# Performance work log

Measured on AMD Instinct MI355X. Metric: run time of the kernel, lower is better.

The kernel has to match this reference:

```python
import jax, jax.numpy as jnp
from jax import lax
import numpy as np

NF = 64      # feature channels
G = 8        # mask groups
NBR = 3      # top-k neighbors
PATCH = 7    # correlation patch size (patches[0])
CORK = 3     # correlation / unfold kernel size
PAD_COR = 1  # (CORK-1)//2
PAD_S = 4    # PAD_COR + (PATCH-1)//2
ADD = 6      # 2*PAD_S - CORK + 1
B, H, W = 4, 96, 96


def leaky(x):
    return jnp.where(x >= 0, x, 0.1 * x)


def _conv(x, w, b, pad):
    y = lax.conv_general_dilated(x, w, (1, 1), [(pad[0], pad[0]), (pad[1], pad[1])],
                                 dimension_numbers=('NCHW', 'OIHW', 'NCHW'))
    return y + b[None, :, None, None]


def _normalize(x, eps=1e-12):
    n = jnp.sqrt(jnp.sum(x * x, axis=1, keepdims=True))
    return x / jnp.maximum(n, eps)


def _correlation(f1, f2):
    # spatial-correlation-sampler: kernel=3, patch=7, stride=1, pad=1, dilations=1
    # out[b, ph*7+pw, i, j] = sum_{c,u,v} f1p[b,c,i+u,j+v] * f2p[b,c,i+u+ph-3, j+v+pw-3]
    # (unnormalized; only topk indices are consumed downstream, so any positive
    #  constant scale is irrelevant)
    Bx, C, Hx, Wx = f1.shape
    f1p = jnp.pad(f1, ((0, 0), (0, 0), (PAD_COR, PAD_COR), (PAD_COR, PAD_COR)))
    f2p = jnp.pad(f2, ((0, 0), (0, 0), (PAD_S, PAD_S), (PAD_S, PAD_S)))
    outs = []
    for ph in range(PATCH):
        for pw in range(PATCH):
            s = jnp.sum(f1p * f2p[:, :, ph:ph + Hx + 2, pw:pw + Wx + 2], axis=1)  # [B,H+2,W+2]
            o = sum(s[:, u:u + Hx, v:v + Wx] for u in range(CORK) for v in range(CORK))
            outs.append(o)
    return jnp.stack(outs, axis=1)  # [B, 49, H, W]


def setup_inputs() -> dict:
    key = jax.random.key(0)
    ks = jax.random.split(key, 16)

    def wt(k, shape):
        fan_in = shape[1] * shape[2] * shape[3]
        return jax.random.normal(k, shape, jnp.float32) * (1.0 / np.sqrt(fan_in))

    return {
        'ref_fea_l': jax.random.normal(ks[0], (B, NF, H, W), jnp.float32),
        'w1': wt(ks[1], (NF, NF * 2, 3, 3)), 'b1': jnp.zeros((NF,), jnp.float32),
        'w2': wt(ks[2], (NF, NF, 3, 3)),     'b2': jnp.zeros((NF,), jnp.float32),
        'w3': wt(ks[3], (NF, NF, 7, 1)),     'b3': jnp.zeros((NF,), jnp.float32),
        'w4': wt(ks[4], (NF, NF, 1, 7)),     'b4': jnp.zeros((NF,), jnp.float32),
        'wm': wt(ks[5], (G * CORK ** 2, NF, 3, 3)), 'bm': jnp.zeros((G * CORK ** 2,), jnp.float32),
        'wnn': wt(ks[6], (NF, NF * NBR, 3, 3)), 'bnn': jnp.zeros((NF,), jnp.float32),
        'wf': wt(ks[7], (NF, NF * 2, 3, 3)),    'bf': jnp.zeros((NF,), jnp.float32),
    }


def reference(ref_fea_l, w1, b1, w2, b2, w3, b3, w4, b4, wm, bm, wnn, bnn, wf, bf):
    Bx, C, Hx, Wx = ref_fea_l.shape
    nbr_fea = ref_fea_l  # aliased in the original forward

    # mask branch
    x = jnp.concatenate([nbr_fea, ref_fea_l], axis=1)
    x = leaky(_conv(x, w1, b1, (1, 1)))
    x = leaky(_conv(x, w2, b2, (1, 1)))
    x = leaky(_conv(x, w3, b3, (3, 0)))
    x = leaky(_conv(x, w4, b4, (0, 3)))
    mask = _conv(x, wm, bm, (1, 1)).reshape(Bx, G, 1, CORK ** 2, Hx, Wx)

    # correlation + topk neighbor displacements
    nref = _normalize(ref_fea_l)
    corr = _correlation(nref, nref)                     # [B,49,H,W]
    _, idx = lax.top_k(corr.transpose(0, 2, 3, 1), NBR)  # [B,H,W,NBR]

    # flat indices into the (H+6)x(W+6) unfold grid
    ph = idx // PATCH
    pw = idx % PATCH
    yy = jnp.arange(Hx)[:, None, None]
    xx = jnp.arange(Wx)[None, :, None]
    flat = ((ph + yy) * (Wx + ADD) + (pw + xx)).reshape(Bx, Hx * Wx * NBR)

    # unfold (im2col) of nbr features with pad 4, then gather chosen 3x3 patches
    nbr_pad = jnp.pad(nbr_fea, ((0, 0), (0, 0), (PAD_S, PAD_S), (PAD_S, PAD_S)))
    patches = lax.conv_general_dilated_patches(nbr_pad, (CORK, CORK), (1, 1), 'VALID',
                                               dimension_numbers=('NCHW', 'OIHW', 'NCHW'))
    pl = patches.reshape(Bx, C * CORK ** 2, -1).transpose(0, 2, 1)  # [B, (H+6)(W+6), C*9]
    gath = jnp.take_along_axis(pl, flat[:, :, None], axis=1)        # [B, HW*NBR, C*9]
    gath = gath.reshape(Bx * Hx * Wx, NBR * C, CORK, CORK)

    # conv over gathered patches then modulated mask-weighted reduce
    g = leaky(_conv(gath, wnn, bnn, (1, 1)))                         # [BHW, C, 3, 3]
    g = g.reshape(Bx, Hx, Wx, C, CORK ** 2).transpose(0, 3, 4, 1, 2)
    g = g.reshape(Bx, G, C // G, CORK ** 2, Hx, Wx)
    agg = leaky(jnp.sum(g * mask, axis=3).reshape(Bx, C, Hx, Wx))

    out = leaky(_conv(jnp.concatenate([ref_fea_l, agg], axis=1), wf, bf, (1, 1)))
    return out
```

## Files before the change

### kernel.cpp

```cpp
#include <hip/hip_runtime.h>
#include <hip/hip_bf16.h>

constexpr int BATCH = 4;
constexpr int H = 96, W = 96, HW = H * W;
constexpr int NBR = 3;

using bf16x8 = __attribute__((ext_vector_type(8))) short;
using f32x4 = __attribute__((ext_vector_type(4))) float;

static __device__ __forceinline__ float leakyf(float x) {
    return x >= 0.f ? x : 0.1f * x;
}

static __device__ __forceinline__ short f2bf(float x) {
    __hip_bfloat16 h = __float2bfloat16(x);
    return *reinterpret_cast<short*>(&h);
}

static __device__ __forceinline__ float bf2f(short s) {
    __hip_bfloat16 h = *reinterpret_cast<__hip_bfloat16*>(&s);
    return __bfloat162float(h);
}

__global__ __launch_bounds__(256) void k_pre(const float* __restrict__ ref,
                                             short* __restrict__ reft,
                                             float* __restrict__ nrn) {
    int p = blockIdx.x * 256 + threadIdx.x;
    if (p >= BATCH * HW) return;
    int b = p / HW, ij = p % HW;
    const float* src = ref + b * 64 * HW + ij;
    float v[64];
    float ss = 0.f;
#pragma unroll
    for (int c = 0; c < 64; ++c) {
        v[c] = src[c * HW];
        ss += v[c] * v[c];
    }
    float inv = 1.f / fmaxf(sqrtf(ss), 1e-12f);
    short* rd = reft + (size_t)p * 64;
#pragma unroll
    for (int cc = 0; cc < 8; ++cc) {
        bf16x8 o;
#pragma unroll
        for (int j = 0; j < 8; ++j) o[j] = f2bf(v[cc * 8 + j]);
        *(bf16x8*)(rd + cc * 8) = o;
    }
    float* nd = nrn + b * 64 * HW + ij;
#pragma unroll
    for (int c = 0; c < 64; ++c) nd[c * HW] = v[c] * inv;
}

__global__ void k_prep(const float* __restrict__ src, short* __restrict__ dst,
                       int OC, int ICt, int ICsrc, int KH, int KW, int NT,
                       int fold, int total) {
    int i = blockIdx.x * 256 + threadIdx.x;
    if (i >= total) return;
    int e = i & 7, l = (i >> 3) & 63;
    int rest = i >> 9;
    int nt = rest % NT;
    rest /= NT;
    int ICK = ICt >> 5;
    int kk = rest % ICK;
    int tap = rest / ICK;
    int ic = kk * 32 + (l >> 4) * 8 + e;
    int oc = nt * 16 + (l & 15);
    int u = tap / KW, v = tap % KW;
    float val = 0.f;
    if (oc < OC) {
        val = src[((oc * ICsrc + ic) * KH + u) * KW + v];
        if (fold) val += src[((oc * ICsrc + 64 + ic) * KH + u) * KW + v];
    }
    dst[i] = f2bf(val);
}

template <int KH, int KW, int IC, int OC, int OMODE, bool BLDS, int NSPL>
__global__ __launch_bounds__(512) void k_cmfma(
    const short* __restrict__ inA, const short* __restrict__ inB,
    const short* __restrict__ Bp, const float* __restrict__ bias,
    void* __restrict__ outp) {
    constexpr int TI = 8, TJ = 32;
    constexpr int PH = (KH - 1) / 2, PW = (KW - 1) / 2;
    constexpr int LR = TI + KH - 1, LC = TJ + KW - 1;
    constexpr int ICB = IC * 2;
    constexpr int LS = (ICB == 128) ? 7 : 8;
    constexpr int ICK = IC / 32;
    constexpr int NTF = (OC + 15) / 16;
    constexpr int NTb = NTF / NSPL;
    constexpr int TAPS = KH * KW;
    constexpr int NOCT = ICB / 16;
    __shared__ char Xs[LR * LC * ICB];
    __shared__ short Bs[BLDS ? TAPS * ICK * NTb * 512 : 8];
    const int tj0 = blockIdx.x * TJ, ti0 = blockIdx.y * TI;
    const int b = blockIdx.z / NSPL;
    const int nt0 = (blockIdx.z % NSPL) * NTb;
    const int tid = threadIdx.x;
    if (BLDS) {
        for (int u2 = tid; u2 < TAPS * ICK * NTb * 64; u2 += 512) {
            int l2 = u2 & 63;
            int rest = u2 >> 6;
            int nt = rest % NTb;
            int qk = rest / NTb;
            ((bf16x8*)Bs)[u2] = ((const bf16x8*)Bp)[(qk * NTF + nt0 + nt) * 64 + l2];
        }
    }
    for (int u2 = tid; u2 < LR * LC * NOCT; u2 += 512) {
        int oct = u2 % NOCT;
        int hp = u2 / NOCT;
        int hr = hp / LC, hc = hp % LC;
        int gi = ti0 + hr - PH, gj = tj0 + hc - PW;
        bf16x8 v = {};
        if (gi >= 0 && gi < H && gj >= 0 && gj < W) {
            const short* s = (oct < 8) ? inA : inB;
            v = *(const bf16x8*)(s + (size_t)(b * HW + gi * W + gj) * 64 +
                                 (oct & 7) * 8);
        }
        int byte = hp * ICB + oct * 16;
        byte ^= ((byte >> LS) & 7) << 4;
        *(bf16x8*)(Xs + byte) = v;
    }
    __syncthreads();
    const int wave = tid >> 6, l = tid & 63;
    const int r = l & 15, q = l >> 4;
    const int mt0 = wave * 2;
    int p0 = mt0 * 16 + r, p1 = p0 + 16;
    int li0 = p0 >> 5, lj0 = p0 & 31, li1 = p1 >> 5, lj1 = p1 & 31;
    f32x4 acc[2][NTb] = {};
#pragma unroll
    for (int t = 0; t < TAPS; ++t) {
        const int u = t / KW, v = t % KW;
        int hp0 = (li0 + u) * LC + (lj0 + v);
        int hp1 = (li1 + u) * LC + (lj1 + v);
#pragma unroll
        for (int kk = 0; kk < ICK; ++kk) {
            int ab0 = hp0 * ICB + kk * 64 + q * 16;
            ab0 ^= ((ab0 >> LS) & 7) << 4;
            int ab1 = hp1 * ICB + kk * 64 + q * 16;
            ab1 ^= ((ab1 >> LS) & 7) << 4;
            bf16x8 a0 = *(const bf16x8*)(Xs + ab0);
            bf16x8 a1 = *(const bf16x8*)(Xs + ab1);
            const short* bbase =
                BLDS ? (const short*)Bs + (t * ICK + kk) * NTb * 512 + l * 8
                     : Bp + ((t * ICK + kk) * NTF + nt0) * 512 + l * 8;
#pragma unroll
            for (int nt = 0; nt < NTb; ++nt) {
                bf16x8 bv = *(const bf16x8*)(bbase + nt * 512);
                acc[0][nt] =
                    __builtin_amdgcn_mfma_f32_16x16x32_bf16(a0, bv, acc[0][nt], 0, 0, 0);
                acc[1][nt] =
                    __builtin_amdgcn_mfma_f32_16x16x32_bf16(a1, bv, acc[1][nt], 0, 0, 0);
            }
        }
    }
    const int col = l & 15;
#pragma unroll
    for (int mt = 0; mt < 2; ++mt)
#pragma unroll
        for (int nt = 0; nt < NTb; ++nt) {
            int oc = (nt0 + nt) * 16 + col;
            float bs = (oc < OC) ? bias[oc] : 0.f;
#pragma unroll
            for (int j = 0; j < 4; ++j) {
                int p = (mt0 + mt) * 16 + q * 4 + j;
                int gi = ti0 + (p >> 5), gj = tj0 + (p & 31);
                float val = acc[mt][nt][j] + bs;
                if (OMODE == 0) {
                    val = leakyf(val);
                    *((short*)outp + (size_t)(b * HW + gi * W + gj) * 64 + oc) =
                        f2bf(val);
                } else if (OMODE == 1) {
                    if (oc < 72)
                        *((short*)outp + (size_t)(b * HW + gi * W + gj) * 72 + oc) =
                            f2bf(val);
                } else {
                    val = leakyf(val);
                    *((float*)outp + (size_t)(b * 64 + oc) * HW + gi * W + gj) = val;
                }
            }
        }
}

__global__ void k_corr_sym(const float* __restrict__ nr, float* __restrict__ S) {
    int idx = blockIdx.x * 256 + threadIdx.x;
    if (idx >= BATCH * 25 * 98 * 98) return;
    int x = idx % 98;
    int y = (idx / 98) % 98;
    int d = (idx / (98 * 98)) % 25;
    int b = idx / (98 * 98 * 25);
    int dy = d / 7, dx = d % 7;
    int f1i = y - 1, f1j = x - 1;
    int f2i = y + dy - 4, f2j = x + dx - 4;
    float r = 0.f;
    if (f1i >= 0 && f1i < H && f1j >= 0 && f1j < W && f2i >= 0 && f2i < H &&
        f2j >= 0 && f2j < W) {
        const float* p1 = nr + b * 64 * HW + f1i * W + f1j;
        const float* p2 = nr + b * 64 * HW + f2i * W + f2j;
#pragma unroll 16
        for (int c = 0; c < 64; ++c) r = fmaf(p1[c * HW], p2[c * HW], r);
    }
    S[((size_t)(b * 49 + d)) * (98 * 98) + y * 98 + x] = r;
    if (d < 24) {
        int y2 = y + dy - 3, x2 = x + dx - 3;
        if (y2 >= 0 && y2 < 98 && x2 >= 0 && x2 < 98)
            S[((size_t)(b * 49 + 48 - d)) * (98 * 98) + y2 * 98 + x2] = r;
    }
}

__global__ void k_topk(const float* __restrict__ S, int* __restrict__ idx3) {
    int p = blockIdx.x * 256 + threadIdx.x;
    if (p >= BATCH * HW) return;
    int b = p / HW, i = (p % HW) / W, j = p % W;
    float v0 = -1e30f, v1 = -1e30f, v2 = -1e30f;
    int d0 = 0, d1 = 0, d2 = 0;
    for (int d = 0; d < 49; ++d) {
        const float* s = S + ((b * 49 + d) * 98 + i) * 98 + j;
        float v = 0.f;
#pragma unroll
        for (int u = 0; u < 3; ++u)
#pragma unroll
            for (int vv = 0; vv < 3; ++vv) v += s[u * 98 + vv];
        if (v > v0) {
            v2 = v1; d2 = d1; v1 = v0; d1 = d0; v0 = v; d0 = d;
        } else if (v > v1) {
            v2 = v1; d2 = d1; v1 = v; d1 = d;
        } else if (v > v2) {
            v2 = v; d2 = d;
        }
    }
    idx3[p * 3 + 0] = d0;
    idx3[p * 3 + 1] = d1;
    idx3[p * 3 + 2] = d2;
}

__global__ void k_bswz2(const float* __restrict__ wnn, short* __restrict__ B2) {
    int i = blockIdx.x * 256 + threadIdx.x;
    if (i >= 4 * 3 * 2 * 9 * 512) return;
    int e = i & 7, l = (i >> 3) & 63;
    int t = (i >> 9) % 9;
    int h2 = (i / (512 * 9)) % 2;
    int n = (i / (512 * 9 * 2)) % 3;
    int nt = i / (512 * 9 * 2 * 3);
    int oc = nt * 16 + (l & 15);
    int c = h2 * 32 + (l >> 4) * 8 + e;
    int u = t / 3, v = t % 3;
    B2[i] = f2bf(wnn[((oc * 192 + n * 64 + c) * 3 + u) * 3 + v]);
}

__global__ __launch_bounds__(512, 4) void k_agg_mfma(
    const short* __restrict__ refT, const int* __restrict__ idx3,
    const short* __restrict__ B2, const float* __restrict__ bnn,
    const short* __restrict__ maskT, short* __restrict__ agg) {
    constexpr int PX = 32;
    constexpr int BUFB = 2 * 18 * 64 * 8 * 2;
    __shared__ short A_lds[2 * 2 * 18 * 64 * 8];
    __shared__ int sd[PX][NBR];
    const int p0 = blockIdx.x * PX;
    const int b = p0 / HW;
    const int i0 = (p0 % HW) / W;
    const int j0 = p0 % W;
    const int tid = threadIdx.x;
    if (tid < PX * NBR)
        sd[tid / NBR][tid % NBR] = idx3[(p0 + tid / NBR) * NBR + tid % NBR];
    __syncthreads();

    bf16x8 greg[5];
    int gbyte[5];

    auto LD = [&](int n, int buf) {
#pragma unroll
        for (int i = 0; i < 5; ++i) {
            int u = tid + i * 512;
            if (u < PX * 9 * 8) {
                int oct = u & 7;
                int q = u >> 3;
                int rs = q % 9;
                int px = q / 9;
                int d = sd[px][n];
                int gi = i0 + d / 7 + rs / 3 - 4;
                int gj = j0 + px + d % 7 + rs % 3 - 4;
                bf16x8 val = {};
                if (gi >= 0 && gi < H && gj >= 0 && gj < W)
                    val = *(const bf16x8*)(refT +
                                           (size_t)(b * HW + gi * W + gj) * 64 +
                                           oct * 8);
                int kkl = rs * 2 + (oct >> 2);
                int chunk = ((px >> 4) * 18 + kkl) * 64 + (oct & 3) * 16 + (px & 15);
                int byte = buf * BUFB + (chunk << 4);
                byte ^= ((byte >> 8) & 7) << 4;
                greg[i] = val;
                gbyte[i] = byte;
            } else {
                gbyte[i] = -1;
            }
        }
    };
    auto WR = [&]() {
#pragma unroll
        for (int i = 0; i < 5; ++i)
            if (gbyte[i] >= 0) *(bf16x8*)((char*)A_lds + gbyte[i]) = greg[i];
    };

    const int wave = tid >> 6;
    const int lane = tid & 63;
    const int w = wave & 3;
    const int half = wave >> 2;
    f32x4 acc[9] = {};
    const short* Bw = B2 + (size_t)w * (3 * 2 * 9 * 512) + lane * 8;

    auto COMPUTE = [&](int n, int buf) {
#pragma unroll
        for (int h2 = 0; h2 < 2; ++h2) {
            const short* bb = Bw + (n * 2 + h2) * 9 * 512;
            bf16x8 bv[9];
#pragma unroll
            for (int t = 0; t < 9; ++t) bv[t] = *(const bf16x8*)(bb + t * 512);
#pragma unroll
            for (int rs = 0; rs < 9; ++rs) {
                int kkl = rs * 2 + h2;
                int ab = buf * BUFB + ((((half * 18 + kkl) << 6) + lane) << 4);
                ab ^= ((ab >> 8) & 7) << 4;
                bf16x8 a = *(const bf16x8*)((char*)A_lds + ab);
#pragma unroll
                for (int t = 0; t < 9; ++t) {
                    const int y = rs / 3 - t / 3 + 1;
                    const int x = rs % 3 - t % 3 + 1;
                    if (y >= 0 && y < 3 && x >= 0 && x < 3)
                        acc[y * 3 + x] = __builtin_amdgcn_mfma_f32_16x16x32_bf16(
                            a, bv[t], acc[y * 3 + x], 0, 0, 0);
                }
            }
        }
    };

    LD(0, 0);
    WR();
    LD(1, 1);
    __syncthreads();
    COMPUTE(0, 0);
    WR();
    LD(2, 0);
    __syncthreads();
    COMPUTE(1, 1);
    WR();
    __syncthreads();
    COMPUTE(2, 0);

    const int oc = w * 16 + (lane & 15);
    const float bn = bnn[oc];
    const int mrow = (lane >> 4) * 4;
#pragma unroll
    for (int j = 0; j < 4; ++j) {
        int px = half * 16 + mrow + j;
        int ij = i0 * W + j0 + px;
        const short* mb = maskT + (size_t)(b * HW + ij) * 72 + (oc >> 3) * 9;
        float sacc = 0.f;
#pragma unroll
        for (int yx = 0; yx < 9; ++yx) {
            float gv = leakyf(acc[yx][j] + bn);
            sacc += gv * bf2f(mb[yx]);
        }
        agg[(size_t)(b * HW + ij) * 64 + oc] = f2bf(leakyf(sacc));
    }
}

extern "C" void kernel_launch(void* const* d_in, const int* in_sizes, int n_in,
                              void* d_out, int out_size, void* d_ws,
                              size_t ws_size, hipStream_t stream) {
    const float* ref = (const float*)d_in[0];
    const float* w1 = (const float*)d_in[1];
    const float* b1 = (const float*)d_in[2];
    const float* w2 = (const float*)d_in[3];
    const float* b2 = (const float*)d_in[4];
    const float* w3 = (const float*)d_in[5];
    const float* b3 = (const float*)d_in[6];
    const float* w4 = (const float*)d_in[7];
    const float* b4 = (const float*)d_in[8];
    const float* wm = (const float*)d_in[9];
    const float* bm = (const float*)d_in[10];
    const float* wnn = (const float*)d_in[11];
    const float* bnn = (const float*)d_in[12];
    const float* wf = (const float*)d_in[13];
    const float* bf = (const float*)d_in[14];

    char* ws = (char*)d_ws;
    constexpr size_t O_NRN = 0;
    constexpr size_t O_S = O_NRN + (size_t)BATCH * HW * 64 * 4;
    constexpr size_t O_REFT = O_S + (size_t)BATCH * 49 * 98 * 98 * 4;
    constexpr size_t O_X1 = O_REFT + (size_t)BATCH * HW * 64 * 2;
    constexpr size_t O_X2 = O_X1 + (size_t)BATCH * HW * 64 * 2;
    constexpr size_t O_MASKT = O_X2 + (size_t)BATCH * HW * 64 * 2;
    constexpr size_t O_IDX = O_MASKT + (size_t)BATCH * HW * 72 * 2;
    constexpr size_t O_P1 = O_IDX + (size_t)BATCH * HW * 3 * 4;
    constexpr size_t O_P2 = O_P1 + 73728 * 2;
    constexpr size_t O_P3 = O_P2 + 73728 * 2;
    constexpr size_t O_P4 = O_P3 + 28672 * 2;
    constexpr size_t O_PM = O_P4 + 28672 * 2;
    constexpr size_t O_PF = O_PM + 46080 * 2;

    float* NRN = (float*)(ws + O_NRN);
    float* S = (float*)(ws + O_S);
    short* BSWZ2 = (short*)(ws + O_S);
    short* REFT = (short*)(ws + O_REFT);
    short* X1 = (short*)(ws + O_X1);
    short* X2 = (short*)(ws + O_X2);
    short* MASKT = (short*)(ws + O_MASKT);
    int* IDX = (int*)(ws + O_IDX);
    short* P1 = (short*)(ws + O_P1);
    short* P2 = (short*)(ws + O_P2);
    short* P3 = (short*)(ws + O_P3);
    short* P4 = (short*)(ws + O_P4);
    short* PM = (short*)(ws + O_PM);
    short* PF = (short*)(ws + O_PF);

    k_pre<<<(BATCH * HW + 255) / 256, 256, 0, stream>>>(ref, REFT, NRN);
    k_prep<<<144, 256, 0, stream>>>(w1, P1, 64, 64, 128, 3, 3, 4, 1, 36864);
    k_prep<<<144, 256, 0, stream>>>(w2, P2, 64, 64, 64, 3, 3, 4, 0, 36864);
    k_prep<<<112, 256, 0, stream>>>(w3, P3, 64, 64, 64, 7, 1, 4, 0, 28672);
    k_prep<<<112, 256, 0, stream>>>(w4, P4, 64, 64, 64, 1, 7, 4, 0, 28672);
    k_prep<<<180, 256, 0, stream>>>(wm, PM, 72, 64, 64, 3, 3, 5, 0, 46080);
    k_prep<<<288, 256, 0, stream>>>(wf, PF, 64, 128, 128, 3, 3, 4, 0, 73728);

    dim3 cgrid2(3, 12, BATCH * 2);
    dim3 cgrid1(3, 12, BATCH);
    k_cmfma<3, 3, 64, 64, 0, true, 2><<<cgrid2, 512, 0, stream>>>(REFT, nullptr, P1, b1, X1);
    k_cmfma<3, 3, 64, 64, 0, true, 2><<<cgrid2, 512, 0, stream>>>(X1, nullptr, P2, b2, X2);
    k_cmfma<7, 1, 64, 64, 0, true, 2><<<cgrid2, 512, 0, stream>>>(X2, nullptr, P3, b3, X1);
    k_cmfma<1, 7, 64, 64, 0, true, 2><<<cgrid2, 512, 0, stream>>>(X1, nullptr, P4, b4, X2);
    k_cmfma<3, 3, 64, 72, 1, true, 1><<<cgrid1, 512, 0, stream>>>(X2, nullptr, PM, bm, MASKT);

    for (int b = 0; b < BATCH; ++b)
        hipMemsetAsync(S + ((size_t)(b * 49 + 25)) * 98 * 98,
                       0, (size_t)24 * 98 * 98 * 4, stream);
    k_corr_sym<<<(BATCH * 25 * 98 * 98 + 255) / 256, 256, 0, stream>>>(NRN, S);
    k_topk<<<BATCH * HW / 256, 256, 0, stream>>>(S, IDX);

    k_bswz2<<<432, 256, 0, stream>>>(wnn, BSWZ2);

    k_agg_mfma<<<BATCH * HW / 32, 512, 0, stream>>>(REFT, IDX, BSWZ2, bnn, MASKT, X1);

    k_cmfma<3, 3, 128, 64, 2, false, 1><<<cgrid1, 512, 0, stream>>>(REFT, X1, PF, bf, d_out);
}
```

Measured before the change: 219.6 us.

## Stage gathered neighbor patches directly into LDS via global_load_lds

Swaps the register-staged gather (global load into VGPRs, then ds_write with XOR swizzle) in the aggregation MFMA kernel for direct global-to-LDS loads. The lane-to-chunk mapping is remapped so each wave writes contiguous 1KB rows while still matching the compute-side swizzled reads. Out-of-bounds taps now read from a zeroed 16-byte pad buffer instead of using a predicated zero. The aim is to free VGPRs and cut the LDS write instructions. The price is a reordered pipeline (the third stage is issued after a barrier) and reliance on barriers to drain the async loads.

```diff
diff --git a/kernel.cpp b/kernel.cpp
--- a/kernel.cpp
+++ b/kernel.cpp
@@ -248,9 +248,10 @@
 __global__ __launch_bounds__(512, 4) void k_agg_mfma(
     const short* __restrict__ refT, const int* __restrict__ idx3,
     const short* __restrict__ B2, const float* __restrict__ bnn,
-    const short* __restrict__ maskT, short* __restrict__ agg) {
+    const short* __restrict__ maskT, const short* __restrict__ zpad,
+    short* __restrict__ agg) {
     constexpr int PX = 32;
-    constexpr int BUFB = 2 * 18 * 64 * 8 * 2;
+    constexpr int BUFB = 36864;
     __shared__ short A_lds[2 * 2 * 18 * 64 * 8];
     __shared__ int sd[PX][NBR];
     const int p0 = blockIdx.x * PX;
@@ -258,49 +259,36 @@
     const int i0 = (p0 % HW) / W;
     const int j0 = p0 % W;
     const int tid = threadIdx.x;
+    const int wave = tid >> 6;
+    const int lane = tid & 63;
     if (tid < PX * NBR)
         sd[tid / NBR][tid % NBR] = idx3[(p0 + tid / NBR) * NBR + tid % NBR];
     __syncthreads();
 
-    bf16x8 greg[5];
-    int gbyte[5];
-
-    auto LD = [&](int n, int buf) {
-#pragma unroll
-        for (int i = 0; i < 5; ++i) {
-            int u = tid + i * 512;
-            if (u < PX * 9 * 8) {
-                int oct = u & 7;
-                int q = u >> 3;
-                int rs = q % 9;
-                int px = q / 9;
-                int d = sd[px][n];
-                int gi = i0 + d / 7 + rs / 3 - 4;
-                int gj = j0 + px + d % 7 + rs % 3 - 4;
-                bf16x8 val = {};
-                if (gi >= 0 && gi < H && gj >= 0 && gj < W)
-                    val = *(const bf16x8*)(refT +
-                                           (size_t)(b * HW + gi * W + gj) * 64 +
-                                           oct * 8);
-                int kkl = rs * 2 + (oct >> 2);
-                int chunk = ((px >> 4) * 18 + kkl) * 64 + (oct & 3) * 16 + (px & 15);
-                int byte = buf * BUFB + (chunk << 4);
-                byte ^= ((byte >> 8) & 7) << 4;
-                greg[i] = val;
-                gbyte[i] = byte;
-            } else {
-                gbyte[i] = -1;
-            }
+    auto STAGE = [&](int n, int buf) {
+        for (int r2 = wave; r2 < 36; r2 += 8) {
+            int kkl = r2 % 18;
+            int ph = r2 / 18;
+            int rs = kkl >> 1;
+            int oh = kkl & 1;
+            int c = lane ^ (((lane >> 4) & 3) | (((buf * 36 + r2) & 1) << 2));
+            int oct = oh * 4 + (c >> 4);
+            int px = ph * 16 + (c & 15);
+            int d = sd[px][n];
+            int gi = i0 + d / 7 + rs / 3 - 4;
+            int gj = j0 + px + d % 7 + rs % 3 - 4;
+            const short* src = (gi >= 0 && gi < H && gj >= 0 && gj < W)
+                                   ? refT + (size_t)(b * HW + gi * W + gj) * 64 +
+                                         oct * 8
+                                   : zpad;
+            __builtin_amdgcn_global_load_lds(
+                (const __attribute__((address_space(1))) void*)src,
+                (__attribute__((address_space(3))) void*)((char*)A_lds +
+                                                          buf * BUFB + r2 * 1024),
+                16, 0, 0);
         }
     };
-    auto WR = [&]() {
-#pragma unroll
-        for (int i = 0; i < 5; ++i)
-            if (gbyte[i] >= 0) *(bf16x8*)((char*)A_lds + gbyte[i]) = greg[i];
-    };
-
-    const int wave = tid >> 6;
-    const int lane = tid & 63;
+
     const int w = wave & 3;
     const int half = wave >> 2;
     f32x4 acc[9] = {};
@@ -331,16 +319,13 @@
         }
     };
 
-    LD(0, 0);
-    WR();
-    LD(1, 1);
+    STAGE(0, 0);
+    STAGE(1, 1);
     __syncthreads();
     COMPUTE(0, 0);
-    WR();
-    LD(2, 0);
     __syncthreads();
+    STAGE(2, 0);
     COMPUTE(1, 1);
-    WR();
     __syncthreads();
     COMPUTE(2, 0);
 
@@ -395,6 +380,7 @@
     constexpr size_t O_P4 = O_P3 + 28672 * 2;
     constexpr size_t O_PM = O_P4 + 28672 * 2;
     constexpr size_t O_PF = O_PM + 46080 * 2;
+    constexpr size_t O_ZP = O_PF + 73728 * 2;
 
     float* NRN = (float*)(ws + O_NRN);
     float* S = (float*)(ws + O_S);
@@ -410,6 +396,7 @@
     short* P4 = (short*)(ws + O_P4);
     short* PM = (short*)(ws + O_PM);
     short* PF = (short*)(ws + O_PF);
+    short* ZPAD = (short*)(ws + O_ZP);
 
     k_pre<<<(BATCH * HW + 255) / 256, 256, 0, stream>>>(ref, REFT, NRN);
     k_prep<<<144, 256, 0, stream>>>(w1, P1, 64, 64, 128, 3, 3, 4, 1, 36864);
@@ -430,12 +417,14 @@
     for (int b = 0; b < BATCH; ++b)
         hipMemsetAsync(S + ((size_t)(b * 49 + 25)) * 98 * 98,
                        0, (size_t)24 * 98 * 98 * 4, stream);
+    hipMemsetAsync(ZPAD, 0, 16, stream);
     k_corr_sym<<<(BATCH * 25 * 98 * 98 + 255) / 256, 256, 0, stream>>>(NRN, S);
     k_topk<<<BATCH * HW / 256, 256, 0, stream>>>(S, IDX);
 
     k_bswz2<<<432, 256, 0, stream>>>(wnn, BSWZ2);
 
-    k_agg_mfma<<<BATCH * HW / 32, 512, 0, stream>>>(REFT, IDX, BSWZ2, bnn, MASKT, X1);
+    k_agg_mfma<<<BATCH * HW / 32, 512, 0, stream>>>(REFT, IDX, BSWZ2, bnn, MASKT,
+                                                    ZPAD, X1);
 
     k_cmfma<3, 3, 128, 64, 2, false, 1><<<cgrid1, 512, 0, stream>>>(REFT, X1, PF, bf, d_out);
 }
```

New measurement: 209.0 us. -4.8%, faster.
